# Kernel tuning notes

Measured on AMD Instinct MI355X. Metric: run time of the kernel, lower is better.

The kernel has to match this reference:

```python
import jax, jax.numpy as jnp
import numpy as np

N = 100000      # nodes
E = 1600000     # edges
IN, H, OUT = 128, 128, 64
FUSION_W = 0.5


def setup_inputs() -> dict:
    key = jax.random.key(0)
    ks = jax.random.split(key, 10)
    x = jax.random.normal(ks[0], (N, IN), dtype=jnp.float32)
    edge_index = jax.random.randint(ks[1], (2, E), 0, N, dtype=jnp.int32)

    def lin(k, fi, fo):
        return jax.random.normal(k, (fi, fo), dtype=jnp.float32) / np.float32(np.sqrt(fi))

    return {
        "x": x,
        "edge_index": edge_index,
        "gnn_W1": lin(ks[2], IN, H),  "gnn_b1": jnp.zeros((H,), jnp.float32),
        "gnn_W2": lin(ks[3], H, OUT), "gnn_b2": jnp.zeros((OUT,), jnp.float32),
        "mlp_W1": lin(ks[4], IN, H),  "mlp_b1": jnp.zeros((H,), jnp.float32),
        "mlp_W2": lin(ks[5], H, OUT), "mlp_b2": jnp.zeros((OUT,), jnp.float32),
    }


def _gcn_conv(x, W, b, src, dst, deg_inv_sqrt, deg_inv):
    # GCNConv: x' = D^{-1/2} (A + I) D^{-1/2} (x W) + b, deg counts self-loops
    h = x @ W                                     # [N, F_out]
    norm = deg_inv_sqrt[src] * deg_inv_sqrt[dst]  # [E]
    agg = jax.ops.segment_sum(h[src] * norm[:, None], dst, num_segments=N)
    # self-loop contribution has norm 1/deg
    return agg + h * deg_inv[:, None] + b


def reference(x, edge_index, gnn_W1, gnn_b1, gnn_W2, gnn_b2,
              mlp_W1, mlp_b1, mlp_W2, mlp_b2):
    src, dst = edge_index[0], edge_index[1]
    # in-degree including self-loops (PyG GCNConv default add_self_loops=True)
    deg = 1.0 + jax.ops.segment_sum(jnp.ones((E,), jnp.float32), dst, num_segments=N)
    deg_inv_sqrt = jax.lax.rsqrt(deg)
    deg_inv = 1.0 / deg

    # GNN branch (dropout is identity in eval mode)
    h = jax.nn.relu(_gcn_conv(x, gnn_W1, gnn_b1, src, dst, deg_inv_sqrt, deg_inv))
    z_gnn = _gcn_conv(h, gnn_W2, gnn_b2, src, dst, deg_inv_sqrt, deg_inv)

    # MLP branch
    z_mlp = jax.nn.relu(x @ mlp_W1 + mlp_b1) @ mlp_W2 + mlp_b2

    return FUSION_W * z_gnn + (1.0 - FUSION_W) * z_mlp
```

## Files before the change

### kernel.cpp

```cpp
#include <hip/hip_runtime.h>
#include <hip/hip_fp16.h>

static constexpr int IN_F = 128;
static constexpr int FCAP = 6144;

typedef _Float16 half8 __attribute__((ext_vector_type(8)));
typedef _Float16 half4 __attribute__((ext_vector_type(4)));
typedef float f32x4 __attribute__((ext_vector_type(4)));
typedef float f32x2 __attribute__((ext_vector_type(2)));

__device__ inline void acc_fp8x8(uint2 u, f32x2* a) {
    a[0] += __builtin_amdgcn_cvt_pk_f32_fp8(u.x, false);
    a[1] += __builtin_amdgcn_cvt_pk_f32_fp8(u.x, true);
    a[2] += __builtin_amdgcn_cvt_pk_f32_fp8(u.y, false);
    a[3] += __builtin_amdgcn_cvt_pk_f32_fp8(u.y, true);
}
__device__ inline void acc_fp8x4(unsigned u, f32x2* a) {
    a[0] += __builtin_amdgcn_cvt_pk_f32_fp8(u, false);
    a[1] += __builtin_amdgcn_cvt_pk_f32_fp8(u, true);
}
__device__ inline void fp8x8_to_f32(uint2 u, float* f) {
    f32x2 a0 = __builtin_amdgcn_cvt_pk_f32_fp8(u.x, false);
    f32x2 a1 = __builtin_amdgcn_cvt_pk_f32_fp8(u.x, true);
    f32x2 a2 = __builtin_amdgcn_cvt_pk_f32_fp8(u.y, false);
    f32x2 a3 = __builtin_amdgcn_cvt_pk_f32_fp8(u.y, true);
    f[0] = a0[0]; f[1] = a0[1]; f[2] = a1[0]; f[3] = a1[1];
    f[4] = a2[0]; f[5] = a2[1]; f[6] = a3[0]; f[7] = a3[1];
}
__device__ inline void fp8x4_to_f32(unsigned u, float* f) {
    f32x2 a0 = __builtin_amdgcn_cvt_pk_f32_fp8(u, false);
    f32x2 a1 = __builtin_amdgcn_cvt_pk_f32_fp8(u, true);
    f[0] = a0[0]; f[1] = a0[1]; f[2] = a1[0]; f[3] = a1[1];
}
__device__ inline unsigned char f32_to_fp8(float v) {
    return (unsigned char)__builtin_amdgcn_cvt_pk_fp8_f32(v, v, 0, false);
}


__global__ __launch_bounds__(1024) void kb_count(const int* __restrict__ dst,
                                                 int* __restrict__ bcount, int E) {
    __shared__ int cnt[16][512];
    const int tid = threadIdx.x;
    const int wv  = tid >> 6;
    for (int i = tid; i < 16 * 512; i += 1024) (&cnt[0][0])[i] = 0;
    __syncthreads();
#pragma unroll
    for (int q = 0; q < 8; ++q) {
        int i = blockIdx.x * 8192 + q * 1024 + tid;
        if (i < E) atomicAdd(&cnt[wv][dst[i] >> 8], 1);
    }
    __syncthreads();
    if (tid < 512) {
        int run = 0;
#pragma unroll
        for (int w = 0; w < 16; ++w) run += cnt[w][tid];
        if (run > 0) atomicAdd(&bcount[tid], run);
    }
}

__global__ __launch_bounds__(512) void k_scanb(const int* __restrict__ bcount,
                                               int* __restrict__ bbase,
                                               int* __restrict__ bcursor, int NB) {
    __shared__ int s[512];
    const int tid = threadIdx.x;
    int v = (tid < NB) ? bcount[tid] : 0;
    s[tid] = v;
    __syncthreads();
    int inc = v;
#pragma unroll
    for (int off = 1; off < 512; off <<= 1) {
        int add = (tid >= off) ? s[tid - off] : 0;
        __syncthreads();
        s[tid] = inc = inc + add;
        __syncthreads();
    }
    if (tid < NB) { bbase[tid] = inc - v; bcursor[tid] = inc - v; }
    if (tid == NB - 1) bbase[NB] = inc;
}

__global__ __launch_bounds__(1024) void kb_move(const int* __restrict__ src,
                                                const int* __restrict__ dst,
                                                int* __restrict__ bcursor,
                                                unsigned* __restrict__ recs, int E) {
    __shared__ int cnt[16][512];
    __shared__ int gbase[512];
    const int tid = threadIdx.x;
    const int wv  = tid >> 6;
    for (int i = tid; i < 16 * 512; i += 1024) (&cnt[0][0])[i] = 0;
    __syncthreads();

    int bq[8];
    unsigned rq[8];
#pragma unroll
    for (int q = 0; q < 8; ++q) {
        int i = blockIdx.x * 8192 + q * 1024 + tid;
        if (i < E) {
            int d = dst[i];
            int s = src[i];
            bq[q] = d >> 8;
            rq[q] = (unsigned)(((d & 255) << 17) | s);
            atomicAdd(&cnt[wv][bq[q]], 1);
        } else {
            bq[q] = -1;
            rq[q] = 0u;
        }
    }
    __syncthreads();
    if (tid < 512) {
        int run = 0;
#pragma unroll
        for (int w = 0; w < 16; ++w) {
            int t = cnt[w][tid];
            cnt[w][tid] = run;
            run += t;
        }
        gbase[tid] = (run > 0) ? atomicAdd(&bcursor[tid], run) : 0;
    }
    __syncthreads();
#pragma unroll
    for (int q = 0; q < 8; ++q) {
        if (bq[q] >= 0) {
            int p = gbase[bq[q]] + atomicAdd(&cnt[wv][bq[q]], 1);
            recs[p] = rq[q];
        }
    }
}

__global__ __launch_bounds__(512) void kb_fill_lds(const unsigned* __restrict__ recs,
                                                   const int* __restrict__ bbase,
                                                   int* __restrict__ row_ptr,
                                                   float* __restrict__ dis,
                                                   int* __restrict__ csr, int n) {
    __shared__ int hist[256];
    __shared__ int sc[256];
    __shared__ int base[257];
    __shared__ int cur[256];
    __shared__ int stage[FCAP];
    const int tid   = threadIdx.x;
    const int b     = blockIdx.x;
    const int s     = bbase[b], e = bbase[b + 1];
    const int nbase = b << 8;

    if (tid < 256) hist[tid] = 0;
    __syncthreads();
    for (int i = s + tid; i < e; i += 512)
        atomicAdd(&hist[recs[i] >> 17], 1);
    __syncthreads();

    const int v = (tid < 256) ? hist[tid] : 0;
    if (tid < 256) sc[tid] = v;
    __syncthreads();
    int inc = v;
#pragma unroll
    for (int off = 1; off < 256; off <<= 1) {
        int add = (tid >= off && tid < 256) ? sc[tid - off] : 0;
        __syncthreads();
        if (tid < 256) sc[tid] = inc = inc + add;
        __syncthreads();
    }
    if (tid < 256) {
        const int excl = inc - v;
        base[tid] = excl;
        if (tid == 255) base[256] = inc;
        cur[tid] = 0;

        const int idx = nbase + tid;
        if (idx < n) {
            row_ptr[idx] = s + excl;
            dis[idx] = rsqrtf(1.0f + (float)v);
        }
        if (idx == n) row_ptr[n] = s + excl;
        if (tid == 255 && nbase + 256 == n) row_ptr[n] = s + inc;
    }
    __syncthreads();

    for (int i = s + tid; i < e; i += 512) {
        unsigned r = recs[i];
        int dl = (int)(r >> 17);
        int slot = base[dl] + atomicAdd(&cur[dl], 1);
        int sr = (int)(r & 0x1FFFFu);
        if (slot < FCAP) stage[slot] = sr;
        else csr[s + slot] = sr;
    }
    __syncthreads();

    const int total = e - s;
    const int lim = total < FCAP ? total : FCAP;
    for (int i = tid; i < lim; i += 512)
        csr[s + i] = stage[i];
}

__global__ __launch_bounds__(256) void k_prep_w(const float* __restrict__ gW1,
                                                const float* __restrict__ mW1,
                                                const float* __restrict__ mW2,
                                                const float* __restrict__ gW2,
                                                _Float16* __restrict__ tg1,
                                                _Float16* __restrict__ tm1,
                                                _Float16* __restrict__ tm2,
                                                _Float16* __restrict__ tg2) {
    int i = blockIdx.x * 256 + threadIdx.x;
    if (i < 16384)      { int j = i;         int f = j >> 7, k = j & 127; tg1[j] = (_Float16)gW1[k * 128 + f]; }
    else if (i < 32768) { int j = i - 16384; int f = j >> 7, k = j & 127; tm1[j] = (_Float16)mW1[k * 128 + f]; }
    else if (i < 40960) { int j = i - 32768; int f = j >> 7, k = j & 127; tm2[j] = (_Float16)mW2[k * 64 + f]; }
    else if (i < 49152) { int j = i - 40960; int f = j >> 7, k = j & 127; tg2[j] = (_Float16)gW2[k * 64 + f]; }
}

__global__ __launch_bounds__(256) void k_dual_mfma(const float* __restrict__ x,
                                                   const _Float16* __restrict__ tg1,
                                                   const _Float16* __restrict__ tm1,
                                                   const _Float16* __restrict__ tm2,
                                                   const float* __restrict__ b1,
                                                   const float* __restrict__ b2,
                                                   const float* __restrict__ dis,
                                                   unsigned char* __restrict__ h1,
                                                   _Float16* __restrict__ z, int nrows) {
    __shared__ _Float16 As[64 * 128];
    __shared__ _Float16 Ws[64 * 128];
    _Float16* Ms = As;
    const int tid  = threadIdx.x;
    const int row0 = blockIdx.x * 64;

#pragma unroll
    for (int p = 0; p < 4; ++p) {
        int sid = p * 256 + tid;
        int r = sid >> 4, s = sid & 15;
        int gr = row0 + r;
        uint4 v = make_uint4(0, 0, 0, 0);
        if (gr < nrows) {
            const float4 f0 = *reinterpret_cast<const float4*>(x + (size_t)gr * 128 + s * 8);
            const float4 f1 = *reinterpret_cast<const float4*>(x + (size_t)gr * 128 + s * 8 + 4);
            _Float16 t[8] = {(_Float16)f0.x, (_Float16)f0.y, (_Float16)f0.z, (_Float16)f0.w,
                             (_Float16)f1.x, (_Float16)f1.y, (_Float16)f1.z, (_Float16)f1.w};
            v = *reinterpret_cast<uint4*>(t);
        }
        *reinterpret_cast<uint4*>(&As[r * 128 + ((s ^ (r & 7)) * 8)]) = v;
    }

    const int lane = tid & 63;
    const int wv   = tid >> 6;
    const int mrow = wv * 16 + (lane & 15);
    const int kg   = lane >> 4;
    const int grow = row0 + wv * 16 + kg * 4;

    auto stageW = [&](const _Float16* Wt, int wbase) {
#pragma unroll
        for (int p = 0; p < 4; ++p) {
            int sid = p * 256 + tid;
            int r = sid >> 4, s = sid & 15;
            uint4 v = *reinterpret_cast<const uint4*>(Wt + (size_t)(wbase + r) * 128 + s * 8);
            *reinterpret_cast<uint4*>(&Ws[r * 128 + ((s ^ (r & 7)) * 8)]) = v;
        }
    };

    stageW(tg1, 0);
    __syncthreads();

    half8 a[4];
#pragma unroll
    for (int kk = 0; kk < 4; ++kk)
        a[kk] = *reinterpret_cast<const half8*>(&As[mrow * 128 + (((kk * 4 + kg) ^ (mrow & 7)) * 8)]);

    float dvals[4];
#pragma unroll
    for (int j = 0; j < 4; ++j)
        dvals[j] = (grow + j < nrows) ? dis[grow + j] : 0.f;

#pragma unroll
    for (int half = 0; half < 2; ++half) {
        if (half == 1) {
            __syncthreads();
            stageW(tg1, 64);
            __syncthreads();
        }
#pragma unroll
        for (int ct = 0; ct < 4; ++ct) {
            const int ncol = half * 64 + ct * 16 + (lane & 15);
            const int wrow = ncol & 63;
            f32x4 acc = {0.f, 0.f, 0.f, 0.f};
#pragma unroll
            for (int kk = 0; kk < 4; ++kk) {
                half8 b = *reinterpret_cast<const half8*>(&Ws[wrow * 128 + (((kk * 4 + kg) ^ (wrow & 7)) * 8)]);
                acc = __builtin_amdgcn_mfma_f32_16x16x32_f16(a[kk], b, acc, 0, 0, 0);
            }
#pragma unroll
            for (int j = 0; j < 4; ++j)
                if (grow + j < nrows)
                    h1[(size_t)(grow + j) * 128 + ncol] = f32_to_fp8(acc[j] * dvals[j]);
        }
    }
    __syncthreads();

#pragma unroll
    for (int half = 0; half < 2; ++half) {
        stageW(tm1, half * 64);
        __syncthreads();
#pragma unroll
        for (int ct = 0; ct < 4; ++ct) {
            const int ncol = half * 64 + ct * 16 + (lane & 15);
            const int wrow = ncol & 63;
            f32x4 acc = {0.f, 0.f, 0.f, 0.f};
#pragma unroll
            for (int kk = 0; kk < 4; ++kk) {
                half8 b = *reinterpret_cast<const half8*>(&Ws[wrow * 128 + (((kk * 4 + kg) ^ (wrow & 7)) * 8)]);
                acc = __builtin_amdgcn_mfma_f32_16x16x32_f16(a[kk], b, acc, 0, 0, 0);
            }
            const float bias = b1[ncol];
#pragma unroll
            for (int j = 0; j < 4; ++j) {
                int r = wv * 16 + kg * 4 + j;
                float v = fmaxf((float)acc[j] + bias, 0.f);
                Ms[r * 128 + (((ncol >> 3) ^ (r & 7)) * 8) + (ncol & 7)] = (_Float16)v;
            }
        }
        __syncthreads();
    }

    stageW(tm2, 0);
    __syncthreads();

    half8 am[4];
#pragma unroll
    for (int kk = 0; kk < 4; ++kk)
        am[kk] = *reinterpret_cast<const half8*>(&Ms[mrow * 128 + (((kk * 4 + kg) ^ (mrow & 7)) * 8)]);

#pragma unroll
    for (int ct = 0; ct < 4; ++ct) {
        const int ncol = ct * 16 + (lane & 15);
        f32x4 acc = {0.f, 0.f, 0.f, 0.f};
#pragma unroll
        for (int kk = 0; kk < 4; ++kk) {
            half8 b = *reinterpret_cast<const half8*>(&Ws[ncol * 128 + (((kk * 4 + kg) ^ (ncol & 7)) * 8)]);
            acc = __builtin_amdgcn_mfma_f32_16x16x32_f16(am[kk], b, acc, 0, 0, 0);
        }
        const float bias = b2[ncol];
#pragma unroll
        for (int j = 0; j < 4; ++j)
            if (grow + j < nrows)
                z[(size_t)(grow + j) * 64 + ncol] = (_Float16)((float)acc[j] + bias);
    }
}

__global__ __launch_bounds__(256) void k_mm64(const _Float16* __restrict__ A,
                                              const _Float16* __restrict__ Wt,
                                              const float* __restrict__ dis,
                                              unsigned char* __restrict__ C, int nrows) {
    __shared__ _Float16 As[64 * 128];
    __shared__ _Float16 Ws[64 * 128];
    const int tid  = threadIdx.x;
    const int row0 = blockIdx.x * 64;

#pragma unroll
    for (int p = 0; p < 4; ++p) {
        int sid = p * 256 + tid;
        int r = sid >> 4, s = sid & 15;
        int gr = row0 + r;
        uint4 v = make_uint4(0, 0, 0, 0);
        if (gr < nrows) v = *reinterpret_cast<const uint4*>(A + (size_t)gr * 128 + s * 8);
        *reinterpret_cast<uint4*>(&As[r * 128 + ((s ^ (r & 7)) * 8)]) = v;
    }
#pragma unroll
    for (int p = 0; p < 4; ++p) {
        int sid = p * 256 + tid;
        int r = sid >> 4, s = sid & 15;
        uint4 v = *reinterpret_cast<const uint4*>(Wt + (size_t)r * 128 + s * 8);
        *reinterpret_cast<uint4*>(&Ws[r * 128 + ((s ^ (r & 7)) * 8)]) = v;
    }
    __syncthreads();

    const int lane = tid & 63;
    const int wv   = tid >> 6;
    const int mrow = wv * 16 + (lane & 15);
    const int kg   = lane >> 4;
    const int grow = row0 + wv * 16 + kg * 4;

    half8 a[4];
#pragma unroll
    for (int kk = 0; kk < 4; ++kk)
        a[kk] = *reinterpret_cast<const half8*>(&As[mrow * 128 + (((kk * 4 + kg) ^ (mrow & 7)) * 8)]);

    float dvals[4];
#pragma unroll
    for (int j = 0; j < 4; ++j)
        dvals[j] = (grow + j < nrows) ? dis[grow + j] : 0.f;

#pragma unroll
    for (int ct = 0; ct < 4; ++ct) {
        const int ncol = ct * 16 + (lane & 15);
        f32x4 acc = {0.f, 0.f, 0.f, 0.f};
#pragma unroll
        for (int kk = 0; kk < 4; ++kk) {
            half8 b = *reinterpret_cast<const half8*>(&Ws[ncol * 128 + (((kk * 4 + kg) ^ (ncol & 7)) * 8)]);
            acc = __builtin_amdgcn_mfma_f32_16x16x32_f16(a[kk], b, acc, 0, 0, 0);
        }
#pragma unroll
        for (int j = 0; j < 4; ++j)
            if (grow + j < nrows)
                C[(size_t)(grow + j) * 64 + ncol] = f32_to_fp8(acc[j] * dvals[j]);
    }
}

__global__ __launch_bounds__(256) void k_agg1(const int* __restrict__ rp,
                                              const int* __restrict__ csr,
                                              const float* __restrict__ dis,
                                              const unsigned char* __restrict__ h1,
                                              const float* __restrict__ b,
                                              _Float16* __restrict__ out, int n) {
    const int tid  = threadIdx.x;
    const int node = blockIdx.x * 4 + (tid >> 6);
    if (node >= n) return;
    const int lane = tid & 63;
    const int g    = lane >> 4;
    const int c0   = (lane & 15) * 8;
    const int start = rp[node], end = rp[node + 1];

    f32x2 acc[4] = {{0.f, 0.f}, {0.f, 0.f}, {0.f, 0.f}, {0.f, 0.f}};

    int j = start + g;
    for (; j + 12 < end; j += 16) {
        int s0 = csr[j];
        int s1 = csr[j + 4];
        int s2 = csr[j + 8];
        int s3 = csr[j + 12];
        uint2 u0 = *reinterpret_cast<const uint2*>(h1 + (size_t)s0 * 128 + c0);
        uint2 u1 = *reinterpret_cast<const uint2*>(h1 + (size_t)s1 * 128 + c0);
        uint2 u2 = *reinterpret_cast<const uint2*>(h1 + (size_t)s2 * 128 + c0);
        uint2 u3 = *reinterpret_cast<const uint2*>(h1 + (size_t)s3 * 128 + c0);
        acc_fp8x8(u0, acc);
        acc_fp8x8(u1, acc);
        acc_fp8x8(u2, acc);
        acc_fp8x8(u3, acc);
    }
    for (; j < end; j += 4) {
        int s0 = csr[j];
        uint2 u0 = *reinterpret_cast<const uint2*>(h1 + (size_t)s0 * 128 + c0);
        acc_fp8x8(u0, acc);
    }

    float av[8] = {acc[0][0], acc[0][1], acc[1][0], acc[1][1],
                   acc[2][0], acc[2][1], acc[3][0], acc[3][1]};
#pragma unroll
    for (int k = 0; k < 8; ++k) {
        av[k] += __shfl_xor(av[k], 16);
        av[k] += __shfl_xor(av[k], 32);
    }

    if (g == 0) {
        const float dd = dis[node];
        uint2 un = *reinterpret_cast<const uint2*>(h1 + (size_t)node * 128 + c0);
        float fn[8];
        fp8x8_to_f32(un, fn);
        const float4 bv0 = *reinterpret_cast<const float4*>(b + c0);
        const float4 bv1 = *reinterpret_cast<const float4*>(b + c0 + 4);
        const float bb[8] = {bv0.x, bv0.y, bv0.z, bv0.w, bv1.x, bv1.y, bv1.z, bv1.w};
        half8 o;
#pragma unroll
        for (int k = 0; k < 8; ++k)
            o[k] = (_Float16)fmaxf(dd * (av[k] + fn[k]) + bb[k], 0.f);
        *reinterpret_cast<half8*>(out + (size_t)node * 128 + c0) = o;
    }
}

__global__ __launch_bounds__(256) void k_agg2(const int* __restrict__ rp,
                                              const int* __restrict__ csr,
                                              const float* __restrict__ dis,
                                              const unsigned char* __restrict__ h2,
                                              const float* __restrict__ b,
                                              const _Float16* __restrict__ zmlp,
                                              float* __restrict__ out, int n) {
    const int tid  = threadIdx.x;
    const int node = blockIdx.x * 4 + (tid >> 6);
    if (node >= n) return;
    const int lane = tid & 63;
    const int g    = lane >> 4;
    const int c0   = (lane & 15) * 4;
    const int start = rp[node], end = rp[node + 1];

    f32x2 acc[2] = {{0.f, 0.f}, {0.f, 0.f}};

    int j = start + g;
    for (; j + 12 < end; j += 16) {
        int s0 = csr[j];
        int s1 = csr[j + 4];
        int s2 = csr[j + 8];
        int s3 = csr[j + 12];
        unsigned u0 = *reinterpret_cast<const unsigned*>(h2 + (size_t)s0 * 64 + c0);
        unsigned u1 = *reinterpret_cast<const unsigned*>(h2 + (size_t)s1 * 64 + c0);
        unsigned u2 = *reinterpret_cast<const unsigned*>(h2 + (size_t)s2 * 64 + c0);
        unsigned u3 = *reinterpret_cast<const unsigned*>(h2 + (size_t)s3 * 64 + c0);
        acc_fp8x4(u0, acc);
        acc_fp8x4(u1, acc);
        acc_fp8x4(u2, acc);
        acc_fp8x4(u3, acc);
    }
    for (; j < end; j += 4) {
        int s0 = csr[j];
        unsigned u0 = *reinterpret_cast<const unsigned*>(h2 + (size_t)s0 * 64 + c0);
        acc_fp8x4(u0, acc);
    }

    float av[4] = {acc[0][0], acc[0][1], acc[1][0], acc[1][1]};
#pragma unroll
    for (int k = 0; k < 4; ++k) {
        av[k] += __shfl_xor(av[k], 16);
        av[k] += __shfl_xor(av[k], 32);
    }

    if (g == 0) {
        const float dd = dis[node];
        unsigned un = *reinterpret_cast<const unsigned*>(h2 + (size_t)node * 64 + c0);
        float fn[4];
        fp8x4_to_f32(un, fn);
        half4 zm = *reinterpret_cast<const half4*>(zmlp + (size_t)node * 64 + c0);
        const float4 bv = *reinterpret_cast<const float4*>(b + c0);
        const float bb[4] = {bv.x, bv.y, bv.z, bv.w};
        float4 o;
        float* op = &o.x;
#pragma unroll
        for (int k = 0; k < 4; ++k)
            op[k] = 0.5f * ((dd * (av[k] + fn[k]) + bb[k]) + (float)zm[k]);
        *reinterpret_cast<float4*>(out + (size_t)node * 64 + c0) = o;
    }
}

extern "C" void kernel_launch(void* const* d_in, const int* in_sizes, int n_in,
                              void* d_out, int out_size, void* d_ws, size_t ws_size,
                              hipStream_t stream) {
    const float* x      = (const float*)d_in[0];
    const int* edge_idx = (const int*)d_in[1];
    const float* gnn_W1 = (const float*)d_in[2];
    const float* gnn_b1 = (const float*)d_in[3];
    const float* gnn_W2 = (const float*)d_in[4];
    const float* gnn_b2 = (const float*)d_in[5];
    const float* mlp_W1 = (const float*)d_in[6];
    const float* mlp_b1 = (const float*)d_in[7];
    const float* mlp_W2 = (const float*)d_in[8];
    const float* mlp_b2 = (const float*)d_in[9];
    float* out = (float*)d_out;

    const int N = in_sizes[0] / IN_F;
    const int E = in_sizes[1] / 2;
    const int* src = edge_idx;
    const int* dst = edge_idx + E;

    const int NB = (N + 255) >> 8;

    char* wp = (char*)d_ws;
    int* row_ptr   = (int*)wp;            wp += ((size_t)N + 4) * sizeof(int);
    int* bbase     = (int*)wp;            wp += 516 * sizeof(int);
    int* bcursor   = (int*)wp;            wp += 512 * sizeof(int);
    int* bcount    = (int*)wp;            wp += 512 * sizeof(int);
    int* csr       = (int*)wp;            wp += (size_t)E * sizeof(int);
    unsigned* recs = (unsigned*)wp;       wp += (size_t)E * sizeof(unsigned);
    float* dis     = (float*)wp;          wp += (size_t)N * sizeof(float);
    _Float16* tg1  = (_Float16*)wp;       wp += 16384 * sizeof(_Float16);
    _Float16* tm1  = (_Float16*)wp;       wp += 16384 * sizeof(_Float16);
    _Float16* tm2  = (_Float16*)wp;       wp += 8192 * sizeof(_Float16);
    _Float16* tg2  = (_Float16*)wp;       wp += 8192 * sizeof(_Float16);
    unsigned char* h1 = (unsigned char*)wp;  wp += (size_t)N * 128;
    _Float16* hmid = (_Float16*)wp;       wp += (size_t)N * 128 * sizeof(_Float16);
    unsigned char* h2 = (unsigned char*)wp;  wp += (size_t)N * 64;
    wp = (char*)(((uintptr_t)wp + 15) & ~(uintptr_t)15);
    _Float16* zmlp = (_Float16*)wp;       wp += (size_t)N * 64 * sizeof(_Float16);

    k_prep_w<<<192, 256, 0, stream>>>(gnn_W1, mlp_W1, mlp_W2, gnn_W2, tg1, tm1, tm2, tg2);

    hipMemsetAsync(bcount, 0, 512 * sizeof(int), stream);
    const int mvblocks = (E + 8191) / 8192;
    kb_count<<<mvblocks, 1024, 0, stream>>>(dst, bcount, E);
    k_scanb<<<1, 512, 0, stream>>>(bcount, bbase, bcursor, NB);
    kb_move<<<mvblocks, 1024, 0, stream>>>(src, dst, bcursor, recs, E);
    kb_fill_lds<<<NB, 512, 0, stream>>>(recs, bbase, row_ptr, dis, csr, N);

    const int gblocks = (N + 63) / 64;
    const int ablocks = (N + 3) / 4;

    k_dual_mfma<<<gblocks, 256, 0, stream>>>(x, tg1, tm1, tm2, mlp_b1, mlp_b2, dis, h1, zmlp, N);

    k_agg1<<<ablocks, 256, 0, stream>>>(row_ptr, csr, dis, h1, gnn_b1, hmid, N);

    k_mm64<<<gblocks, 256, 0, stream>>>(hmid, tg2, dis, h2, N);

    k_agg2<<<ablocks, 256, 0, stream>>>(row_ptr, csr, dis, h2, gnn_b2, zmlp, out, N);
}
```

Measured before the change: 197.5 us.

## Sort CSR neighbors by source range and assign 16 lanes per node in aggregation

The CSR fill kernel now builds a 2048-bin histogram keyed on destination and the source's high bits, so each node's neighbor list is roughly ordered by source range. This should improve gather locality in the aggregation kernels. The two aggregation kernels now give each node one 16-lane group instead of a 64-lane wave with four edge groups, which removes the cross-group shuffle reduction and packs 16 nodes per block. In exchange, per-node edge parallelism drops and the fill kernel uses more LDS, which can lower occupancy.

```diff
diff --git a/kernel.cpp b/kernel.cpp
--- a/kernel.cpp
+++ b/kernel.cpp
@@ -130,55 +130,69 @@
                                                    const int* __restrict__ bbase,
                                                    int* __restrict__ row_ptr,
                                                    float* __restrict__ dis,
-                                                   int* __restrict__ csr, int n) {
-    __shared__ int hist[256];
-    __shared__ int sc[256];
-    __shared__ int base[257];
-    __shared__ int cur[256];
+                                                   int* __restrict__ csr, int n, int E) {
+    __shared__ int hist[2048];
+    __shared__ int wsum[512];
+    __shared__ int base[2048];
+    __shared__ int cur[2048];
     __shared__ int stage[FCAP];
     const int tid   = threadIdx.x;
     const int b     = blockIdx.x;
     const int s     = bbase[b], e = bbase[b + 1];
     const int nbase = b << 8;
 
-    if (tid < 256) hist[tid] = 0;
-    __syncthreads();
-    for (int i = s + tid; i < e; i += 512)
-        atomicAdd(&hist[recs[i] >> 17], 1);
-    __syncthreads();
-
-    const int v = (tid < 256) ? hist[tid] : 0;
-    if (tid < 256) sc[tid] = v;
-    __syncthreads();
-    int inc = v;
-#pragma unroll
-    for (int off = 1; off < 256; off <<= 1) {
-        int add = (tid >= off && tid < 256) ? sc[tid - off] : 0;
-        __syncthreads();
-        if (tid < 256) sc[tid] = inc = inc + add;
-        __syncthreads();
-    }
-    if (tid < 256) {
-        const int excl = inc - v;
-        base[tid] = excl;
-        if (tid == 255) base[256] = inc;
-        cur[tid] = 0;
-
-        const int idx = nbase + tid;
-        if (idx < n) {
-            row_ptr[idx] = s + excl;
-            dis[idx] = rsqrtf(1.0f + (float)v);
-        }
-        if (idx == n) row_ptr[n] = s + excl;
-        if (tid == 255 && nbase + 256 == n) row_ptr[n] = s + inc;
-    }
-    __syncthreads();
-
+    for (int i = tid; i < 2048; i += 512) hist[i] = 0;
+    __syncthreads();
     for (int i = s + tid; i < e; i += 512) {
         unsigned r = recs[i];
         int dl = (int)(r >> 17);
-        int slot = base[dl] + atomicAdd(&cur[dl], 1);
         int sr = (int)(r & 0x1FFFFu);
+        atomicAdd(&hist[(dl << 3) | (sr >> 14)], 1);
+    }
+    __syncthreads();
+
+    const int l0 = hist[tid * 4 + 0];
+    const int l1 = hist[tid * 4 + 1];
+    const int l2 = hist[tid * 4 + 2];
+    const int l3 = hist[tid * 4 + 3];
+    const int tot = l0 + l1 + l2 + l3;
+    wsum[tid] = tot;
+    __syncthreads();
+    int inc = tot;
+#pragma unroll
+    for (int off = 1; off < 512; off <<= 1) {
+        int add = (tid >= off) ? wsum[tid - off] : 0;
+        __syncthreads();
+        wsum[tid] = inc = inc + add;
+        __syncthreads();
+    }
+    int run = inc - tot;
+    base[tid * 4 + 0] = run; cur[tid * 4 + 0] = 0; run += l0;
+    base[tid * 4 + 1] = run; cur[tid * 4 + 1] = 0; run += l1;
+    base[tid * 4 + 2] = run; cur[tid * 4 + 2] = 0; run += l2;
+    base[tid * 4 + 3] = run; cur[tid * 4 + 3] = 0; run += l3;
+    __syncthreads();
+
+    if (tid < 256) {
+        int cnt = 0;
+#pragma unroll
+        for (int q = 0; q < 8; ++q) cnt += hist[tid * 8 + q];
+        const int idx = nbase + tid;
+        if (idx < n) {
+            row_ptr[idx] = s + base[tid * 8];
+            dis[idx] = rsqrtf(1.0f + (float)cnt);
+        }
+        if (idx == n) row_ptr[n] = s + base[tid * 8];
+        if (tid == 255 && nbase + 256 == n) row_ptr[n] = e;
+    }
+    __syncthreads();
+
+    for (int i = s + tid; i < e; i += 512) {
+        unsigned r = recs[i];
+        int dl = (int)(r >> 17);
+        int sr = (int)(r & 0x1FFFFu);
+        int k  = (dl << 3) | (sr >> 14);
+        int slot = base[k] + atomicAdd(&cur[k], 1);
         if (slot < FCAP) stage[slot] = sr;
         else csr[s + slot] = sr;
     }
@@ -406,58 +420,42 @@
                                               const float* __restrict__ b,
                                               _Float16* __restrict__ out, int n) {
     const int tid  = threadIdx.x;
-    const int node = blockIdx.x * 4 + (tid >> 6);
+    const int node = blockIdx.x * 16 + (tid >> 4);
     if (node >= n) return;
-    const int lane = tid & 63;
-    const int g    = lane >> 4;
-    const int c0   = (lane & 15) * 8;
+    const int c0 = (tid & 15) * 8;
     const int start = rp[node], end = rp[node + 1];
 
     f32x2 acc[4] = {{0.f, 0.f}, {0.f, 0.f}, {0.f, 0.f}, {0.f, 0.f}};
 
-    int j = start + g;
-    for (; j + 12 < end; j += 16) {
+    int j = start;
+    for (; j + 1 < end; j += 2) {
         int s0 = csr[j];
-        int s1 = csr[j + 4];
-        int s2 = csr[j + 8];
-        int s3 = csr[j + 12];
+        int s1 = csr[j + 1];
         uint2 u0 = *reinterpret_cast<const uint2*>(h1 + (size_t)s0 * 128 + c0);
         uint2 u1 = *reinterpret_cast<const uint2*>(h1 + (size_t)s1 * 128 + c0);
-        uint2 u2 = *reinterpret_cast<const uint2*>(h1 + (size_t)s2 * 128 + c0);
-        uint2 u3 = *reinterpret_cast<const uint2*>(h1 + (size_t)s3 * 128 + c0);
         acc_fp8x8(u0, acc);
         acc_fp8x8(u1, acc);
-        acc_fp8x8(u2, acc);
-        acc_fp8x8(u3, acc);
-    }
-    for (; j < end; j += 4) {
+    }
+    if (j < end) {
         int s0 = csr[j];
         uint2 u0 = *reinterpret_cast<const uint2*>(h1 + (size_t)s0 * 128 + c0);
         acc_fp8x8(u0, acc);
     }
 
-    float av[8] = {acc[0][0], acc[0][1], acc[1][0], acc[1][1],
-                   acc[2][0], acc[2][1], acc[3][0], acc[3][1]};
-#pragma unroll
-    for (int k = 0; k < 8; ++k) {
-        av[k] += __shfl_xor(av[k], 16);
-        av[k] += __shfl_xor(av[k], 32);
-    }
-
-    if (g == 0) {
-        const float dd = dis[node];
-        uint2 un = *reinterpret_cast<const uint2*>(h1 + (size_t)node * 128 + c0);
-        float fn[8];
-        fp8x8_to_f32(un, fn);
-        const float4 bv0 = *reinterpret_cast<const float4*>(b + c0);
-        const float4 bv1 = *reinterpret_cast<const float4*>(b + c0 + 4);
-        const float bb[8] = {bv0.x, bv0.y, bv0.z, bv0.w, bv1.x, bv1.y, bv1.z, bv1.w};
-        half8 o;
-#pragma unroll
-        for (int k = 0; k < 8; ++k)
-            o[k] = (_Float16)fmaxf(dd * (av[k] + fn[k]) + bb[k], 0.f);
-        *reinterpret_cast<half8*>(out + (size_t)node * 128 + c0) = o;
-    }
+    const float dd = dis[node];
+    uint2 un = *reinterpret_cast<const uint2*>(h1 + (size_t)node * 128 + c0);
+    float fn[8];
+    fp8x8_to_f32(un, fn);
+    const float av[8] = {acc[0][0], acc[0][1], acc[1][0], acc[1][1],
+                         acc[2][0], acc[2][1], acc[3][0], acc[3][1]};
+    const float4 bv0 = *reinterpret_cast<const float4*>(b + c0);
+    const float4 bv1 = *reinterpret_cast<const float4*>(b + c0 + 4);
+    const float bb[8] = {bv0.x, bv0.y, bv0.z, bv0.w, bv1.x, bv1.y, bv1.z, bv1.w};
+    half8 o;
+#pragma unroll
+    for (int k = 0; k < 8; ++k)
+        o[k] = (_Float16)fmaxf(dd * (av[k] + fn[k]) + bb[k], 0.f);
+    *reinterpret_cast<half8*>(out + (size_t)node * 128 + c0) = o;
 }
 
 __global__ __launch_bounds__(256) void k_agg2(const int* __restrict__ rp,
@@ -468,58 +466,42 @@
                                               const _Float16* __restrict__ zmlp,
                                               float* __restrict__ out, int n) {
     const int tid  = threadIdx.x;
-    const int node = blockIdx.x * 4 + (tid >> 6);
+    const int node = blockIdx.x * 16 + (tid >> 4);
     if (node >= n) return;
-    const int lane = tid & 63;
-    const int g    = lane >> 4;
-    const int c0   = (lane & 15) * 4;
+    const int c0 = (tid & 15) * 4;
     const int start = rp[node], end = rp[node + 1];
 
     f32x2 acc[2] = {{0.f, 0.f}, {0.f, 0.f}};
 
-    int j = start + g;
-    for (; j + 12 < end; j += 16) {
+    int j = start;
+    for (; j + 1 < end; j += 2) {
         int s0 = csr[j];
-        int s1 = csr[j + 4];
-        int s2 = csr[j + 8];
-        int s3 = csr[j + 12];
+        int s1 = csr[j + 1];
         unsigned u0 = *reinterpret_cast<const unsigned*>(h2 + (size_t)s0 * 64 + c0);
         unsigned u1 = *reinterpret_cast<const unsigned*>(h2 + (size_t)s1 * 64 + c0);
-        unsigned u2 = *reinterpret_cast<const unsigned*>(h2 + (size_t)s2 * 64 + c0);
-        unsigned u3 = *reinterpret_cast<const unsigned*>(h2 + (size_t)s3 * 64 + c0);
         acc_fp8x4(u0, acc);
         acc_fp8x4(u1, acc);
-        acc_fp8x4(u2, acc);
-        acc_fp8x4(u3, acc);
-    }
-    for (; j < end; j += 4) {
+    }
+    if (j < end) {
         int s0 = csr[j];
         unsigned u0 = *reinterpret_cast<const unsigned*>(h2 + (size_t)s0 * 64 + c0);
         acc_fp8x4(u0, acc);
     }
 
-    float av[4] = {acc[0][0], acc[0][1], acc[1][0], acc[1][1]};
-#pragma unroll
-    for (int k = 0; k < 4; ++k) {
-        av[k] += __shfl_xor(av[k], 16);
-        av[k] += __shfl_xor(av[k], 32);
-    }
-
-    if (g == 0) {
-        const float dd = dis[node];
-        unsigned un = *reinterpret_cast<const unsigned*>(h2 + (size_t)node * 64 + c0);
-        float fn[4];
-        fp8x4_to_f32(un, fn);
-        half4 zm = *reinterpret_cast<const half4*>(zmlp + (size_t)node * 64 + c0);
-        const float4 bv = *reinterpret_cast<const float4*>(b + c0);
-        const float bb[4] = {bv.x, bv.y, bv.z, bv.w};
-        float4 o;
-        float* op = &o.x;
-#pragma unroll
-        for (int k = 0; k < 4; ++k)
-            op[k] = 0.5f * ((dd * (av[k] + fn[k]) + bb[k]) + (float)zm[k]);
-        *reinterpret_cast<float4*>(out + (size_t)node * 64 + c0) = o;
-    }
+    const float dd = dis[node];
+    unsigned un = *reinterpret_cast<const unsigned*>(h2 + (size_t)node * 64 + c0);
+    float fn[4];
+    fp8x4_to_f32(un, fn);
+    const float av[4] = {acc[0][0], acc[0][1], acc[1][0], acc[1][1]};
+    half4 zm = *reinterpret_cast<const half4*>(zmlp + (size_t)node * 64 + c0);
+    const float4 bv = *reinterpret_cast<const float4*>(b + c0);
+    const float bb[4] = {bv.x, bv.y, bv.z, bv.w};
+    float4 o;
+    float* op = &o.x;
+#pragma unroll
+    for (int k = 0; k < 4; ++k)
+        op[k] = 0.5f * ((dd * (av[k] + fn[k]) + bb[k]) + (float)zm[k]);
+    *reinterpret_cast<float4*>(out + (size_t)node * 64 + c0) = o;
 }
 
 extern "C" void kernel_launch(void* const* d_in, const int* in_sizes, int n_in,
@@ -569,10 +551,10 @@
     kb_count<<<mvblocks, 1024, 0, stream>>>(dst, bcount, E);
     k_scanb<<<1, 512, 0, stream>>>(bcount, bbase, bcursor, NB);
     kb_move<<<mvblocks, 1024, 0, stream>>>(src, dst, bcursor, recs, E);
-    kb_fill_lds<<<NB, 512, 0, stream>>>(recs, bbase, row_ptr, dis, csr, N);
+    kb_fill_lds<<<NB, 512, 0, stream>>>(recs, bbase, row_ptr, dis, csr, N, E);
 
     const int gblocks = (N + 63) / 64;
-    const int ablocks = (N + 3) / 4;
+    const int ablocks = (N + 15) / 16;
 
     k_dual_mfma<<<gblocks, 256, 0, stream>>>(x, tg1, tm1, tm2, mlp_b1, mlp_b2, dis, h1, zmlp, N);
 
```

After: 182.7 us. 7.5% less time.
